# Kernel optimization log

Measured on AMD Instinct MI355X. Metric: run time of the kernel, lower is better.

## Reference

```python
import jax, jax.numpy as jnp
import numpy as np

B, S, E, H = 16, 512, 1024, 16
DK = E // H  # 64


def setup_inputs() -> dict:
    key = jax.random.key(0)
    ks = jax.random.split(key, 14)
    s_e = 1.0 / np.sqrt(E)
    s_d = 1.0 / np.sqrt(DK)
    return {
        "inp": jax.random.normal(ks[0], (B, S, E), dtype=jnp.float32),
        # projection linears (torch Linear stored as x @ W + b with W pre-transposed)
        "Wq": jax.random.uniform(ks[1], (E, E), jnp.float32, -s_e, s_e),
        "bq": jax.random.uniform(ks[2], (E,), jnp.float32, -s_e, s_e),
        "Wk": jax.random.uniform(ks[3], (E, E), jnp.float32, -s_e, s_e),
        "bk": jax.random.uniform(ks[4], (E,), jnp.float32, -s_e, s_e),
        "Wv": jax.random.uniform(ks[5], (E, E), jnp.float32, -s_e, s_e),
        "bv": jax.random.uniform(ks[6], (E,), jnp.float32, -s_e, s_e),
        # per-head gating linears
        "Wfq": jax.random.uniform(ks[7], (DK, DK), jnp.float32, -s_d, s_d),
        "bfq": jax.random.uniform(ks[8], (DK,), jnp.float32, -s_d, s_d),
        "Wfk": jax.random.uniform(ks[9], (DK, DK), jnp.float32, -s_d, s_d),
        "bfk": jax.random.uniform(ks[10], (DK,), jnp.float32, -s_d, s_d),
        "Wfg": jax.random.uniform(ks[11], (DK, 2 * DK), jnp.float32, -s_d, s_d),
        "bfg": jax.random.uniform(ks[12], (2 * DK,), jnp.float32, -s_d, s_d),
    }


def _split_heads(x):
    # [B, S, E] -> [B, H, S, DK]
    b, s, _ = x.shape
    return x.reshape(b, s, H, DK).transpose(0, 2, 1, 3)


def reference(inp, Wq, bq, Wk, bk, Wv, bv, Wfq, bfq, Wfk, bfk, Wfg, bfg):
    q = _split_heads(inp @ Wq + bq)  # [B,H,S,DK]
    k = _split_heads(inp @ Wk + bk)
    v = _split_heads(inp @ Wv + bv)

    # gated query/key modulation
    G = (q @ Wfq + bfq) * (k @ Wfk + bfk)          # [B,H,S,DK]
    M = jax.nn.sigmoid(G @ Wfg + bfg)              # [B,H,S,2*DK]
    q = q * M[..., :DK]
    k = k * M[..., DK:]

    scores = jnp.einsum("bhqd,bhkd->bhqk", q, k) / jnp.sqrt(jnp.asarray(DK, q.dtype))
    p_attn = jax.nn.softmax(scores, axis=-1)
    x = jnp.einsum("bhqk,bhkd->bhqd", p_attn, v)   # [B,H,S,DK]
    return x.transpose(0, 2, 1, 3).reshape(inp.shape[0], -1, H * DK)
```

## Files before the change

kernel.cpp:

```cpp
#include <hip/hip_runtime.h>


typedef __bf16 bf16;
typedef __bf16 bf16x8 __attribute__((ext_vector_type(8)));
typedef __bf16 bf16x4 __attribute__((ext_vector_type(4)));
typedef float  f32x4  __attribute__((ext_vector_type(4)));

#define MFMA16(a,b,c) __builtin_amdgcn_mfma_f32_16x16x32_bf16((a),(b),(c),0,0,0)

#define GLL16(gp, lp)                                                          \
  __builtin_amdgcn_global_load_lds(                                            \
      (__attribute__((address_space(1))) void*)(void*)(gp),                    \
      (__attribute__((address_space(3))) void*)(lp), 16, 0, 0)

__global__ __launch_bounds__(256) void k_prep(const float* __restrict__ in,
                                              bf16* __restrict__ Xb,
                                              const float* __restrict__ Wq,
                                              const float* __restrict__ Wk,
                                              const float* __restrict__ Wv,
                                              bf16* __restrict__ WT) {
  __shared__ float tile[32][33];
  const int bx = blockIdx.x, t = threadIdx.x;
  if (bx < 8192) {
    int i = bx * 256 + t;
    float4 v = ((const float4*)in)[i];
    bf16x4 o;
    o[0] = (bf16)v.x; o[1] = (bf16)v.y; o[2] = (bf16)v.z; o[3] = (bf16)v.w;
    ((bf16x4*)Xb)[i] = o;
  } else {
    int r = bx - 8192;
    int mat = r >> 10; r &= 1023;
    int kb = r >> 5, nb = r & 31;
    const float* W = (mat == 0) ? Wq : ((mat == 1) ? Wk : Wv);
    bf16* O = WT + (size_t)mat * (1024 * 1024);
    const int tr = t >> 3, tc = (t & 7) * 4;
    float4 v = *(const float4*)&W[(size_t)(kb * 32 + tr) * 1024 + nb * 32 + tc];
    tile[tr][tc] = v.x; tile[tr][tc + 1] = v.y;
    tile[tr][tc + 2] = v.z; tile[tr][tc + 3] = v.w;
    __syncthreads();
    bf16x4 o;
    o[0] = (bf16)tile[tc][tr];     o[1] = (bf16)tile[tc + 1][tr];
    o[2] = (bf16)tile[tc + 2][tr]; o[3] = (bf16)tile[tc + 3][tr];
    *(bf16x4*)&O[(size_t)(nb * 32 + tr) * 1024 + kb * 32 + tc] = o;
  }
}

__global__ __launch_bounds__(512) void k_proj(const bf16* __restrict__ X,
                                              const bf16* __restrict__ WT,
                                              const float* __restrict__ bq,
                                              const float* __restrict__ bk,
                                              const float* __restrict__ bv,
                                              bf16* __restrict__ qw,
                                              bf16* __restrict__ kw,
                                              bf16* __restrict__ vt) {
  extern __shared__ bf16 lds[];
  bf16* As = lds;
  bf16* Bs = lds + 32768;

  const int tid = threadIdx.x;
  const int m0 = blockIdx.x * 256;
  const int n0 = blockIdx.y * 192;

  const int l = tid & 63, wid = tid >> 6;
  const int wm = wid >> 2, wn = wid & 3;
  const int l4 = l & 15, q8 = l >> 4;
  const int cs0 = (q8 ^ (l4 & 7)) * 8;
  const int arow = (wm * 128 + l4) * 64;
  const int brow = (wn * 48 + l4) * 64;

  const int srow = tid >> 3;
  const int scol = ((tid & 7) ^ (srow & 7)) * 8;
  const bf16* Xs = X + (size_t)(m0 + srow) * 1024 + scol;
  const bf16* Ws = WT + (size_t)(n0 + srow) * 1024 + scol;
  const int ldst = tid * 8;

#define STG_AU(bf, kt, u)                                                      \
  GLL16(Xs + (size_t)(u) * 65536 + (kt) * 64,                                  \
        As + (bf) * 16384 + (u) * 4096 + ldst)
#define STG_BU(bf, kt, u)                                                      \
  GLL16(Ws + (size_t)(u) * 65536 + (kt) * 64,                                  \
        Bs + (bf) * 12288 + (u) * 4096 + ldst)

  f32x4 acc[8][3] = {};
  bf16x8 af[4], bfr[3][2];

#define LDA(bf, qm, kk)                                                        \
  do {                                                                         \
    _Pragma("unroll") for (int m_ = 0; m_ < 4; ++m_)                           \
        af[m_] = *(const bf16x8*)&As[(bf) * 16384 + arow + (qm) * 4096 +       \
                                     m_ * 1024 + (cs0 ^ ((kk) * 32))];         \
  } while (0)
#define LDB6(bf)                                                               \
  do {                                                                         \
    _Pragma("unroll") for (int n_ = 0; n_ < 3; ++n_) {                         \
      bfr[n_][0] = *(const bf16x8*)&Bs[(bf) * 12288 + brow + n_ * 1024 + cs0]; \
      bfr[n_][1] =                                                             \
          *(const bf16x8*)&Bs[(bf) * 12288 + brow + n_ * 1024 + (cs0 ^ 32)];   \
    }                                                                          \
  } while (0)
#define MMQ(qm, kk)                                                            \
  do {                                                                         \
    _Pragma("unroll") for (int m_ = 0; m_ < 4; ++m_)                           \
    _Pragma("unroll") for (int n_ = 0; n_ < 3; ++n_)                           \
        acc[(qm) * 4 + m_][n_] =                                               \
            MFMA16(bfr[n_][kk], af[m_], acc[(qm) * 4 + m_][n_]);               \
  } while (0)
#define PH_PRE                                                                 \
  __builtin_amdgcn_s_barrier();                                                \
  asm volatile("s_waitcnt lgkmcnt(0)" ::: "memory");                           \
  __builtin_amdgcn_s_setprio(1)
#define PH_POST                                                                \
  __builtin_amdgcn_s_setprio(0);                                               \
  __builtin_amdgcn_s_barrier()

  STG_AU(0, 0, 0); STG_AU(0, 0, 1); STG_AU(0, 0, 2); STG_AU(0, 0, 3);
  STG_BU(0, 0, 0); STG_BU(0, 0, 1); STG_BU(0, 0, 2);
  STG_BU(1, 1, 0); STG_BU(1, 1, 1); STG_BU(1, 1, 2);
  asm volatile("s_waitcnt vmcnt(3)" ::: "memory");
  __builtin_amdgcn_s_barrier();

#pragma unroll 1
  for (int i = 0; i < 8; ++i) {
    const int t1 = 2 * i + 1;
    const int t2 = (i < 7) ? 2 * i + 2 : 14;
    const int t3 = (i < 7) ? 2 * i + 3 : 15;
    LDB6(0); LDA(0, 0, 0);
    STG_AU(1, t1, 0); STG_AU(1, t1, 1);
    PH_PRE; MMQ(0, 0); PH_POST;
    LDA(0, 0, 1);
    STG_AU(1, t1, 2); STG_AU(1, t1, 3);
    PH_PRE; MMQ(0, 1); PH_POST;
    LDA(0, 1, 0);
    STG_BU(0, t2, 0); STG_BU(0, t2, 1);
    PH_PRE; MMQ(1, 0); PH_POST;
    LDA(0, 1, 1);
    STG_BU(0, t2, 2);
    PH_PRE; MMQ(1, 1);
    __builtin_amdgcn_s_setprio(0);
    asm volatile("s_waitcnt vmcnt(3)" ::: "memory");
    __builtin_amdgcn_s_barrier();
    LDB6(1); LDA(1, 0, 0);
    STG_AU(0, t2, 0); STG_AU(0, t2, 1);
    PH_PRE; MMQ(0, 0); PH_POST;
    LDA(1, 0, 1);
    STG_AU(0, t2, 2); STG_AU(0, t2, 3);
    PH_PRE; MMQ(0, 1); PH_POST;
    LDA(1, 1, 0);
    STG_BU(1, t3, 0); STG_BU(1, t3, 1);
    PH_PRE; MMQ(1, 0); PH_POST;
    LDA(1, 1, 1);
    STG_BU(1, t3, 2);
    PH_PRE; MMQ(1, 1);
    __builtin_amdgcn_s_setprio(0);
    asm volatile("s_waitcnt vmcnt(3)" ::: "memory");
    __builtin_amdgcn_s_barrier();
  }

#pragma unroll
  for (int mi = 0; mi < 8; ++mi) {
    const int m = m0 + wm * 128 + mi * 16 + l4;
    const int b_ = m >> 9, s = m & 511;
#pragma unroll
    for (int nj = 0; nj < 3; ++nj) {
      const int n = n0 + wn * 48 + nj * 16 + q8 * 4;
      const int mat = n >> 10, nn = n & 1023;
      if (mat == 2) {
        const int h = nn >> 6, d0 = nn & 63;
#pragma unroll
        for (int r = 0; r < 4; ++r) {
          vt[((size_t)(b_ * 16 + h) * 64 + d0 + r) * 512 + s] =
              (bf16)(acc[mi][nj][r] + bv[nn + r]);
        }
      } else {
        const float* bias = (mat == 0) ? bq : bk;
        const float4 bb = *(const float4*)&bias[nn];
        bf16x4 o;
        o[0] = (bf16)(acc[mi][nj][0] + bb.x);
        o[1] = (bf16)(acc[mi][nj][1] + bb.y);
        o[2] = (bf16)(acc[mi][nj][2] + bb.z);
        o[3] = (bf16)(acc[mi][nj][3] + bb.w);
        bf16* dst = (mat == 0) ? qw : kw;
        *(bf16x4*)&dst[(size_t)m * 1024 + nn] = o;
      }
    }
  }
#undef STG_AU
#undef STG_BU
#undef LDA
#undef LDB6
#undef MMQ
#undef PH_PRE
#undef PH_POST
}

__global__ __launch_bounds__(256, 2) void k_gate(bf16* __restrict__ qw,
                                                 bf16* __restrict__ kw,
                                                 const float* __restrict__ Wfq,
                                                 const float* __restrict__ bfq,
                                                 const float* __restrict__ Wfk,
                                                 const float* __restrict__ bfk,
                                                 const float* __restrict__ Wfg,
                                                 const float* __restrict__ bfg) {
  __shared__ __align__(16) char smraw[56320];
  bf16* sWq = (bf16*)smraw;
  bf16* sWk = (bf16*)(smraw + 9216);
  bf16* sWg = (bf16*)(smraw + 18432);
  bf16* sG  = (bf16*)(smraw + 36864);
  float* sb = (float*)(smraw + 55296);
  bf16* Ms  = (bf16*)smraw;
  const int tid = threadIdx.x;

  for (int idx = tid; idx < 4096; idx += 256) {
    int k = idx >> 6, n = idx & 63;
    sWq[n * 72 + k] = (bf16)Wfq[k * 64 + n];
    sWk[n * 72 + k] = (bf16)Wfk[k * 64 + n];
  }
  for (int idx = tid; idx < 8192; idx += 256) {
    int k = idx >> 7, n = idx & 127;
    sWg[n * 72 + k] = (bf16)Wfg[k * 128 + n];
  }
  if (tid < 64) { sb[tid] = bfq[tid]; sb[64 + tid] = bfk[tid]; }
  if (tid < 128) sb[128 + tid] = bfg[tid];
  __syncthreads();

  const int w = tid >> 6, l = tid & 63, l4 = l & 15, q8 = l >> 4;
  const int T0 = blockIdx.x * 128;
  const int rbase = w * 32;

  bf16x8 aq[2][2], ak[2][2];
#pragma unroll
  for (int i = 0; i < 2; ++i)
#pragma unroll
    for (int kk = 0; kk < 2; ++kk) {
      size_t off = (size_t)(T0 + rbase + i * 16 + l4) * 64 + kk * 32 + q8 * 8;
      aq[i][kk] = *(const bf16x8*)&qw[off];
      ak[i][kk] = *(const bf16x8*)&kw[off];
    }

  f32x4 fqc[2][4] = {}, fkc[2][4] = {};
#pragma unroll
  for (int j = 0; j < 4; ++j) {
    bf16x8 bq0 = *(const bf16x8*)&sWq[(j * 16 + l4) * 72 + q8 * 8];
    bf16x8 bq1 = *(const bf16x8*)&sWq[(j * 16 + l4) * 72 + 32 + q8 * 8];
    bf16x8 bk0 = *(const bf16x8*)&sWk[(j * 16 + l4) * 72 + q8 * 8];
    bf16x8 bk1 = *(const bf16x8*)&sWk[(j * 16 + l4) * 72 + 32 + q8 * 8];
#pragma unroll
    for (int i = 0; i < 2; ++i) {
      fqc[i][j] = MFMA16(aq[i][0], bq0, fqc[i][j]);
      fqc[i][j] = MFMA16(aq[i][1], bq1, fqc[i][j]);
      fkc[i][j] = MFMA16(ak[i][0], bk0, fkc[i][j]);
      fkc[i][j] = MFMA16(ak[i][1], bk1, fkc[i][j]);
    }
  }

#pragma unroll
  for (int j = 0; j < 4; ++j) {
    float bqb = sb[j * 16 + l4], bkb = sb[64 + j * 16 + l4];
#pragma unroll
    for (int i = 0; i < 2; ++i)
#pragma unroll
      for (int r = 0; r < 4; ++r) {
        int row = rbase + i * 16 + q8 * 4 + r;
        float g = (fqc[i][j][r] + bqb) * (fkc[i][j][r] + bkb);
        sG[row * 72 + j * 16 + l4] = (bf16)g;
      }
  }
  __syncthreads();

  bf16x8 ag[2][2];
#pragma unroll
  for (int i = 0; i < 2; ++i)
#pragma unroll
    for (int kk = 0; kk < 2; ++kk)
      ag[i][kk] = *(const bf16x8*)&sG[(rbase + i * 16 + l4) * 72 + kk * 32 + q8 * 8];
  f32x4 mc[2][8] = {};
#pragma unroll
  for (int jj = 0; jj < 8; ++jj) {
    bf16x8 bg0 = *(const bf16x8*)&sWg[(jj * 16 + l4) * 72 + q8 * 8];
    bf16x8 bg1 = *(const bf16x8*)&sWg[(jj * 16 + l4) * 72 + 32 + q8 * 8];
#pragma unroll
    for (int i = 0; i < 2; ++i) {
      mc[i][jj] = MFMA16(ag[i][0], bg0, mc[i][jj]);
      mc[i][jj] = MFMA16(ag[i][1], bg1, mc[i][jj]);
    }
  }

  __syncthreads();
#pragma unroll
  for (int jj = 0; jj < 8; ++jj) {
    float bgb = sb[128 + jj * 16 + l4];
#pragma unroll
    for (int i = 0; i < 2; ++i)
#pragma unroll
      for (int r = 0; r < 4; ++r) {
        int row = rbase + i * 16 + q8 * 4 + r;
        float m = mc[i][jj][r] + bgb;
        Ms[row * 136 + jj * 16 + l4] = (bf16)(1.0f / (1.0f + __expf(-m)));
      }
  }
  __syncthreads();

  const float SC = 0.18033688011112042f;
  const int tl = tid >> 1, half = tid & 1;
  bf16* base = (half ? kw : qw) + (size_t)(T0 + tl) * 64;
  const float scl = half ? 1.0f : SC;
#pragma unroll
  for (int c = 0; c < 8; ++c) {
    bf16x8 v = *(const bf16x8*)&base[c * 8];
    bf16x8 m = *(const bf16x8*)&Ms[tl * 136 + half * 64 + c * 8];
    bf16x8 o;
#pragma unroll
    for (int e = 0; e < 8; ++e)
      o[e] = (bf16)((float)v[e] * (float)m[e] * scl);
    *(bf16x8*)&base[c * 8] = o;
  }
}

__global__ __launch_bounds__(256, 2) void k_attn(const bf16* __restrict__ qw,
                                                 const bf16* __restrict__ kw,
                                                 const bf16* __restrict__ vt,
                                                 float* __restrict__ out) {
  __shared__ bf16 Kt[128 * 72];
  __shared__ bf16 Vt[64 * 136];
  __shared__ bf16 Pb[4][32 * 40];
  const int tid = threadIdx.x, w = tid >> 6, l = tid & 63;
  const int l4 = l & 15, q8 = l >> 4;
  const int bx = blockIdx.x;
  const int slot = bx >> 3;
  const int qc = slot & 3;
  const int bh = (bx & 7) + 8 * (slot >> 2);
  const int b_ = bh >> 4, h = bh & 15;
  bf16* Pw = &Pb[w][0];

  bf16x8 qf[2][2];
#pragma unroll
  for (int i = 0; i < 2; ++i)
#pragma unroll
    for (int kk = 0; kk < 2; ++kk) {
      int s = qc * 128 + w * 32 + i * 16 + l4;
      qf[i][kk] = *(const bf16x8*)
          &qw[(((size_t)b_ * 512 + s) * 16 + h) * 64 + kk * 32 + q8 * 8];
    }

  f32x4 o[2][4] = {};
  float mrun[2][4], lrun[2][4];
#pragma unroll
  for (int i = 0; i < 2; ++i)
#pragma unroll
    for (int r = 0; r < 4; ++r) { mrun[i][r] = -3.0e38f; lrun[i][r] = 0.0f; }

  for (int t = 0; t < 4; ++t) {
    __syncthreads();
#pragma unroll
    for (int i = 0; i < 4; ++i) {
      int chunk = i * 256 + tid;
      {
        int key = chunk >> 3, c8 = chunk & 7;
        bf16x8 v = *(const bf16x8*)
            &kw[(((size_t)b_ * 512 + t * 128 + key) * 16 + h) * 64 + c8 * 8];
        *(bf16x8*)&Kt[key * 72 + c8 * 8] = v;
      }
      {
        int d = chunk >> 4, c16 = chunk & 15;
        bf16x8 v = *(const bf16x8*)
            &vt[((size_t)bh * 64 + d) * 512 + t * 128 + c16 * 8];
        *(bf16x8*)&Vt[d * 136 + c16 * 8] = v;
      }
    }
    __syncthreads();

    f32x4 sc[2][8];
    const f32x4 fz = {};
#pragma unroll
    for (int c = 0; c < 8; ++c) {
      bf16x8 kb0 = *(const bf16x8*)&Kt[(c * 16 + l4) * 72 + q8 * 8];
      sc[0][c] = MFMA16(qf[0][0], kb0, fz);
      sc[1][c] = MFMA16(qf[1][0], kb0, fz);
      bf16x8 kb1 = *(const bf16x8*)&Kt[(c * 16 + l4) * 72 + 32 + q8 * 8];
      sc[0][c] = MFMA16(qf[0][1], kb1, sc[0][c]);
      sc[1][c] = MFMA16(qf[1][1], kb1, sc[1][c]);
    }

#pragma unroll
    for (int i = 0; i < 2; ++i) {
      float al[4];
#pragma unroll
      for (int r = 0; r < 4; ++r) {
        float mx = sc[i][0][r];
#pragma unroll
        for (int c = 1; c < 8; ++c) mx = fmaxf(mx, sc[i][c][r]);
        mx = fmaxf(mx, __shfl_xor(mx, 1));
        mx = fmaxf(mx, __shfl_xor(mx, 2));
        mx = fmaxf(mx, __shfl_xor(mx, 4));
        mx = fmaxf(mx, __shfl_xor(mx, 8));
        float mn = fmaxf(mrun[i][r], mx);
        al[r] = exp2f(mrun[i][r] - mn);
        mrun[i][r] = mn;
        float sm = 0.0f;
#pragma unroll
        for (int c = 0; c < 8; ++c) {
          float p = exp2f(sc[i][c][r] - mn);
          sc[i][c][r] = p;
          sm += p;
        }
        sm += __shfl_xor(sm, 1); sm += __shfl_xor(sm, 2);
        sm += __shfl_xor(sm, 4); sm += __shfl_xor(sm, 8);
        lrun[i][r] = lrun[i][r] * al[r] + sm;
      }
#pragma unroll
      for (int f = 0; f < 4; ++f)
#pragma unroll
        for (int r = 0; r < 4; ++r) o[i][f][r] *= al[r];
    }

#pragma unroll
    for (int kk2 = 0; kk2 < 4; ++kk2) {
#pragma unroll
      for (int i = 0; i < 2; ++i)
#pragma unroll
        for (int cc = 0; cc < 2; ++cc) {
          int c = kk2 * 2 + cc;
#pragma unroll
          for (int r = 0; r < 4; ++r)
            Pw[(i * 16 + q8 * 4 + r) * 40 + cc * 16 + l4] = (bf16)sc[i][c][r];
        }
      bf16x8 pa0 = *(const bf16x8*)&Pw[(l4) * 40 + q8 * 8];
      bf16x8 pa1 = *(const bf16x8*)&Pw[(16 + l4) * 40 + q8 * 8];
#pragma unroll
      for (int f = 0; f < 4; ++f) {
        bf16x8 vb = *(const bf16x8*)&Vt[(f * 16 + l4) * 136 + kk2 * 32 + q8 * 8];
        o[0][f] = MFMA16(pa0, vb, o[0][f]);
        o[1][f] = MFMA16(pa1, vb, o[1][f]);
      }
    }
  }

#pragma unroll
  for (int i = 0; i < 2; ++i)
#pragma unroll
    for (int r = 0; r < 4; ++r) {
      int srow = qc * 128 + w * 32 + i * 16 + q8 * 4 + r;
      float inv = 1.0f / lrun[i][r];
#pragma unroll
      for (int f = 0; f < 4; ++f)
        out[(((size_t)b_ * 512 + srow) * 16 + h) * 64 + f * 16 + l4] =
            o[i][f][r] * inv;
    }
}

extern "C" void kernel_launch(void* const* d_in, const int* in_sizes, int n_in,
                              void* d_out, int out_size, void* d_ws,
                              size_t ws_size, hipStream_t stream) {
  (void)in_sizes; (void)n_in; (void)out_size; (void)ws_size;
  const float* inp = (const float*)d_in[0];
  const float* Wq  = (const float*)d_in[1];
  const float* bq  = (const float*)d_in[2];
  const float* Wk  = (const float*)d_in[3];
  const float* bk  = (const float*)d_in[4];
  const float* Wv  = (const float*)d_in[5];
  const float* bv  = (const float*)d_in[6];
  const float* Wfq = (const float*)d_in[7];
  const float* bfq = (const float*)d_in[8];
  const float* Wfk = (const float*)d_in[9];
  const float* bfk = (const float*)d_in[10];
  const float* Wfg = (const float*)d_in[11];
  const float* bfg = (const float*)d_in[12];
  float* out = (float*)d_out;

  static bool s_attr = false;
  if (!s_attr) {
    (void)hipFuncSetAttribute((const void*)k_proj,
                              hipFuncAttributeMaxDynamicSharedMemorySize,
                              114688);
    s_attr = true;
  }

  char* ws = (char*)d_ws;
  bf16* Xb = (bf16*)(ws);
  bf16* WT = (bf16*)(ws + 16777216);
  bf16* qw = (bf16*)(ws + 16777216 + 6291456);
  bf16* kw = qw + 8388608;
  bf16* vt = kw + 8388608;

  k_prep<<<11264, 256, 0, stream>>>(inp, Xb, Wq, Wk, Wv, WT);
  k_proj<<<dim3(32, 16), 512, 114688, stream>>>(Xb, WT, bq, bk, bv, qw, kw, vt);
  k_gate<<<1024, 256, 0, stream>>>(qw, kw, Wfq, bfq, Wfk, bfk, Wfg, bfg);
  k_attn<<<1024, 256, 0, stream>>>(qw, kw, vt, out);
}
```

Before: 259.8 us.

## Retile projection GEMM to 128x192 blocks with 4 waves and 2 blocks per CU

The QKV projection GEMM drops from 256x192 tiles with 8 waves to 128x192 tiles with 4 waves. Each wave now computes a 64x96 sub-tile, and the B-operand staging and wait counts are reworked to match. The grid doubles to 1024 blocks, and LDS per block shrinks so two blocks can share a CU. The goals are better wave balance across CUs and more overlap between blocks, at the cost of reloading A/B data more often across blocks and a higher register demand per wave.

```diff
diff --git a/kernel.cpp b/kernel.cpp
--- a/kernel.cpp
+++ b/kernel.cpp
@@ -45,28 +45,28 @@
   }
 }
 
-__global__ __launch_bounds__(512) void k_proj(const bf16* __restrict__ X,
-                                              const bf16* __restrict__ WT,
-                                              const float* __restrict__ bq,
-                                              const float* __restrict__ bk,
-                                              const float* __restrict__ bv,
-                                              bf16* __restrict__ qw,
-                                              bf16* __restrict__ kw,
-                                              bf16* __restrict__ vt) {
+__global__ __launch_bounds__(256, 2) void k_proj(const bf16* __restrict__ X,
+                                                 const bf16* __restrict__ WT,
+                                                 const float* __restrict__ bq,
+                                                 const float* __restrict__ bk,
+                                                 const float* __restrict__ bv,
+                                                 bf16* __restrict__ qw,
+                                                 bf16* __restrict__ kw,
+                                                 bf16* __restrict__ vt) {
   extern __shared__ bf16 lds[];
   bf16* As = lds;
-  bf16* Bs = lds + 32768;
+  bf16* Bs = lds + 16384;
 
   const int tid = threadIdx.x;
-  const int m0 = blockIdx.x * 256;
+  const int m0 = blockIdx.x * 128;
   const int n0 = blockIdx.y * 192;
 
   const int l = tid & 63, wid = tid >> 6;
-  const int wm = wid >> 2, wn = wid & 3;
+  const int wm = wid >> 1, wn = wid & 1;
   const int l4 = l & 15, q8 = l >> 4;
   const int cs0 = (q8 ^ (l4 & 7)) * 8;
-  const int arow = (wm * 128 + l4) * 64;
-  const int brow = (wn * 48 + l4) * 64;
+  const int arow = (wm * 64 + l4) * 64;
+  const int brow = (wn * 96 + l4) * 64;
 
   const int srow = tid >> 3;
   const int scol = ((tid & 7) ^ (srow & 7)) * 8;
@@ -75,35 +75,33 @@
   const int ldst = tid * 8;
 
 #define STG_AU(bf, kt, u)                                                      \
-  GLL16(Xs + (size_t)(u) * 65536 + (kt) * 64,                                  \
-        As + (bf) * 16384 + (u) * 4096 + ldst)
+  GLL16(Xs + (size_t)(u) * 32768 + (kt) * 64,                                  \
+        As + (bf) * 8192 + (u) * 2048 + ldst)
 #define STG_BU(bf, kt, u)                                                      \
-  GLL16(Ws + (size_t)(u) * 65536 + (kt) * 64,                                  \
-        Bs + (bf) * 12288 + (u) * 4096 + ldst)
-
-  f32x4 acc[8][3] = {};
-  bf16x8 af[4], bfr[3][2];
-
-#define LDA(bf, qm, kk)                                                        \
+  GLL16(Ws + (size_t)(u) * 32768 + (kt) * 64,                                  \
+        Bs + (bf) * 12288 + (u) * 2048 + ldst)
+
+  f32x4 acc[4][6] = {};
+  bf16x8 aa[2], bb0[6], bb1[6];
+
+#define LDA2(bf, qm, kk)                                                       \
   do {                                                                         \
-    _Pragma("unroll") for (int m_ = 0; m_ < 4; ++m_)                           \
-        af[m_] = *(const bf16x8*)&As[(bf) * 16384 + arow + (qm) * 4096 +       \
+    _Pragma("unroll") for (int m_ = 0; m_ < 2; ++m_)                           \
+        aa[m_] = *(const bf16x8*)&As[(bf) * 8192 + arow + (qm) * 2048 +        \
                                      m_ * 1024 + (cs0 ^ ((kk) * 32))];         \
   } while (0)
-#define LDB6(bf)                                                               \
+#define LDB6(bf, kk, arr)                                                      \
   do {                                                                         \
-    _Pragma("unroll") for (int n_ = 0; n_ < 3; ++n_) {                         \
-      bfr[n_][0] = *(const bf16x8*)&Bs[(bf) * 12288 + brow + n_ * 1024 + cs0]; \
-      bfr[n_][1] =                                                             \
-          *(const bf16x8*)&Bs[(bf) * 12288 + brow + n_ * 1024 + (cs0 ^ 32)];   \
-    }                                                                          \
+    _Pragma("unroll") for (int n_ = 0; n_ < 6; ++n_)                           \
+        arr[n_] = *(const bf16x8*)&Bs[(bf) * 12288 + brow + n_ * 1024 +        \
+                                      (cs0 ^ ((kk) * 32))];                    \
   } while (0)
-#define MMQ(qm, kk)                                                            \
+#define MMQ(qm, arr)                                                           \
   do {                                                                         \
-    _Pragma("unroll") for (int m_ = 0; m_ < 4; ++m_)                           \
-    _Pragma("unroll") for (int n_ = 0; n_ < 3; ++n_)                           \
-        acc[(qm) * 4 + m_][n_] =                                               \
-            MFMA16(bfr[n_][kk], af[m_], acc[(qm) * 4 + m_][n_]);               \
+    _Pragma("unroll") for (int m_ = 0; m_ < 2; ++m_)                           \
+    _Pragma("unroll") for (int n_ = 0; n_ < 6; ++n_)                           \
+        acc[(qm) * 2 + m_][n_] =                                               \
+            MFMA16(arr[n_], aa[m_], acc[(qm) * 2 + m_][n_]);                   \
   } while (0)
 #define PH_PRE                                                                 \
   __builtin_amdgcn_s_barrier();                                                \
@@ -115,8 +113,10 @@
 
   STG_AU(0, 0, 0); STG_AU(0, 0, 1); STG_AU(0, 0, 2); STG_AU(0, 0, 3);
   STG_BU(0, 0, 0); STG_BU(0, 0, 1); STG_BU(0, 0, 2);
+  STG_BU(0, 0, 3); STG_BU(0, 0, 4); STG_BU(0, 0, 5);
   STG_BU(1, 1, 0); STG_BU(1, 1, 1); STG_BU(1, 1, 2);
-  asm volatile("s_waitcnt vmcnt(3)" ::: "memory");
+  STG_BU(1, 1, 3); STG_BU(1, 1, 4); STG_BU(1, 1, 5);
+  asm volatile("s_waitcnt vmcnt(6)" ::: "memory");
   __builtin_amdgcn_s_barrier();
 
 #pragma unroll 1
@@ -124,45 +124,45 @@
     const int t1 = 2 * i + 1;
     const int t2 = (i < 7) ? 2 * i + 2 : 14;
     const int t3 = (i < 7) ? 2 * i + 3 : 15;
-    LDB6(0); LDA(0, 0, 0);
+    LDB6(0, 0, bb0); LDA2(0, 0, 0);
     STG_AU(1, t1, 0); STG_AU(1, t1, 1);
-    PH_PRE; MMQ(0, 0); PH_POST;
-    LDA(0, 0, 1);
+    PH_PRE; MMQ(0, bb0); PH_POST;
+    LDB6(0, 1, bb1); LDA2(0, 1, 0);
     STG_AU(1, t1, 2); STG_AU(1, t1, 3);
-    PH_PRE; MMQ(0, 1); PH_POST;
-    LDA(0, 1, 0);
-    STG_BU(0, t2, 0); STG_BU(0, t2, 1);
-    PH_PRE; MMQ(1, 0); PH_POST;
-    LDA(0, 1, 1);
-    STG_BU(0, t2, 2);
-    PH_PRE; MMQ(1, 1);
+    PH_PRE; MMQ(1, bb0); PH_POST;
+    LDA2(0, 0, 1);
+    STG_BU(0, t2, 0); STG_BU(0, t2, 1); STG_BU(0, t2, 2);
+    PH_PRE; MMQ(0, bb1); PH_POST;
+    LDA2(0, 1, 1);
+    STG_BU(0, t2, 3); STG_BU(0, t2, 4); STG_BU(0, t2, 5);
+    PH_PRE; MMQ(1, bb1);
     __builtin_amdgcn_s_setprio(0);
-    asm volatile("s_waitcnt vmcnt(3)" ::: "memory");
+    asm volatile("s_waitcnt vmcnt(6)" ::: "memory");
     __builtin_amdgcn_s_barrier();
-    LDB6(1); LDA(1, 0, 0);
+    LDB6(1, 0, bb0); LDA2(1, 0, 0);
     STG_AU(0, t2, 0); STG_AU(0, t2, 1);
-    PH_PRE; MMQ(0, 0); PH_POST;
-    LDA(1, 0, 1);
+    PH_PRE; MMQ(0, bb0); PH_POST;
+    LDB6(1, 1, bb1); LDA2(1, 1, 0);
     STG_AU(0, t2, 2); STG_AU(0, t2, 3);
-    PH_PRE; MMQ(0, 1); PH_POST;
-    LDA(1, 1, 0);
-    STG_BU(1, t3, 0); STG_BU(1, t3, 1);
-    PH_PRE; MMQ(1, 0); PH_POST;
-    LDA(1, 1, 1);
-    STG_BU(1, t3, 2);
-    PH_PRE; MMQ(1, 1);
+    PH_PRE; MMQ(1, bb0); PH_POST;
+    LDA2(1, 0, 1);
+    STG_BU(1, t3, 0); STG_BU(1, t3, 1); STG_BU(1, t3, 2);
+    PH_PRE; MMQ(0, bb1); PH_POST;
+    LDA2(1, 1, 1);
+    STG_BU(1, t3, 3); STG_BU(1, t3, 4); STG_BU(1, t3, 5);
+    PH_PRE; MMQ(1, bb1);
     __builtin_amdgcn_s_setprio(0);
-    asm volatile("s_waitcnt vmcnt(3)" ::: "memory");
+    asm volatile("s_waitcnt vmcnt(6)" ::: "memory");
     __builtin_amdgcn_s_barrier();
   }
 
 #pragma unroll
-  for (int mi = 0; mi < 8; ++mi) {
-    const int m = m0 + wm * 128 + mi * 16 + l4;
+  for (int mi = 0; mi < 4; ++mi) {
+    const int m = m0 + wm * 64 + mi * 16 + l4;
     const int b_ = m >> 9, s = m & 511;
 #pragma unroll
-    for (int nj = 0; nj < 3; ++nj) {
-      const int n = n0 + wn * 48 + nj * 16 + q8 * 4;
+    for (int nj = 0; nj < 6; ++nj) {
+      const int n = n0 + wn * 96 + nj * 16 + q8 * 4;
       const int mat = n >> 10, nn = n & 1023;
       if (mat == 2) {
         const int h = nn >> 6, d0 = nn & 63;
@@ -186,7 +186,7 @@
   }
 #undef STG_AU
 #undef STG_BU
-#undef LDA
+#undef LDA2
 #undef LDB6
 #undef MMQ
 #undef PH_PRE
@@ -471,7 +471,7 @@
   if (!s_attr) {
     (void)hipFuncSetAttribute((const void*)k_proj,
                               hipFuncAttributeMaxDynamicSharedMemorySize,
-                              114688);
+                              81920);
     s_attr = true;
   }
 
@@ -483,7 +483,7 @@
   bf16* vt = kw + 8388608;
 
   k_prep<<<11264, 256, 0, stream>>>(inp, Xb, Wq, Wk, Wv, WT);
-  k_proj<<<dim3(32, 16), 512, 114688, stream>>>(Xb, WT, bq, bk, bv, qw, kw, vt);
+  k_proj<<<dim3(64, 16), 256, 81920, stream>>>(Xb, WT, bq, bk, bv, qw, kw, vt);
   k_gate<<<1024, 256, 0, stream>>>(qw, kw, Wfq, bfq, Wfk, bfk, Wfg, bfg);
   k_attn<<<1024, 256, 0, stream>>>(qw, kw, vt, out);
 }
```

Result: faster. 246.2 us (-5.2%).
